# Kernel optimization log

Hardware: AMD Instinct MI355X
Metric: run time of the kernel (lower is better)

The kernel has to match this reference:

```python
import jax, jax.numpy as jnp
import numpy as np

H = 768
NH = 12
HD = H // NH
FF = 3072
E = 4
EPS = 1e-12


def _make_expert_params(key):
    ks = jax.random.split(key, 8)
    s = 0.02
    return {
        'wq': jax.random.normal(ks[0], (H, H), jnp.float32) * s,
        'wk': jax.random.normal(ks[1], (H, H), jnp.float32) * s,
        'wv': jax.random.normal(ks[2], (H, H), jnp.float32) * s,
        'wo': jax.random.normal(ks[3], (H, H), jnp.float32) * s,
        'bq': jnp.zeros((H,), jnp.float32),
        'bk': jnp.zeros((H,), jnp.float32),
        'bv': jnp.zeros((H,), jnp.float32),
        'bo': jnp.zeros((H,), jnp.float32),
        'ln1_g': jnp.ones((H,), jnp.float32),
        'ln1_b': jnp.zeros((H,), jnp.float32),
        'w1': jax.random.normal(ks[4], (H, FF), jnp.float32) * s,
        'b1': jnp.zeros((FF,), jnp.float32),
        'w2': jax.random.normal(ks[5], (FF, H), jnp.float32) * s,
        'b2': jnp.zeros((H,), jnp.float32),
        'ln2_g': jnp.ones((H,), jnp.float32),
        'ln2_b': jnp.zeros((H,), jnp.float32),
    }


def setup_inputs() -> dict:
    key = jax.random.key(0)
    k1, k2, kp = jax.random.split(key, 3)
    hidden_states = jax.random.normal(k1, (64, 128, H), jnp.float32)
    attention_mask = jnp.zeros((64, 128), jnp.float32)  # additive mask, 0 = attend
    centers = jax.random.normal(k2, (E, H), jnp.float32)
    pkeys = jax.random.split(kp, E)
    ps = [_make_expert_params(k) for k in pkeys]
    # stack expert params along leading axis for vectorized gather-by-expert
    params = {k: jnp.stack([p[k] for p in ps], axis=0) for k in ps[0]}
    out = {'hidden_states': hidden_states, 'attention_mask': attention_mask, 'centers': centers}
    out.update(params)
    return out


def _layernorm(x, g, b):
    mu = x.mean(-1, keepdims=True)
    var = ((x - mu) ** 2).mean(-1, keepdims=True)
    return (x - mu) * jax.lax.rsqrt(var + EPS) * g + b


def _encoder(x, mask, p):
    # x: [B,S,H], mask: [B,S] additive; p: per-sample expert params (leading dim B)
    B, S, _ = x.shape
    q = jnp.einsum('bsh,bhd->bsd', x, p['wq']) + p['bq'][:, None, :]
    k = jnp.einsum('bsh,bhd->bsd', x, p['wk']) + p['bk'][:, None, :]
    v = jnp.einsum('bsh,bhd->bsd', x, p['wv']) + p['bv'][:, None, :]
    q = q.reshape(B, S, NH, HD)
    k = k.reshape(B, S, NH, HD)
    v = v.reshape(B, S, NH, HD)
    scores = jnp.einsum('bqnd,bknd->bnqk', q, k) / np.sqrt(HD).astype(np.float32)
    scores = scores + mask[:, None, None, :]
    attn = jax.nn.softmax(scores, axis=-1)
    ctx = jnp.einsum('bnqk,bknd->bqnd', attn, v).reshape(B, S, H)
    att_out = jnp.einsum('bsh,bhd->bsd', ctx, p['wo']) + p['bo'][:, None, :]
    att_out = _layernorm(att_out + x, p['ln1_g'][:, None, :], p['ln1_b'][:, None, :])
    ffn = jnp.einsum('bsh,bhf->bsf', att_out, p['w1']) + p['b1'][:, None, :]
    ffn = jax.nn.gelu(ffn)
    ffn = jnp.einsum('bsf,bfh->bsh', ffn, p['w2']) + p['b2'][:, None, :]
    out = _layernorm(att_out + ffn, p['ln2_g'][:, None, :], p['ln2_b'][:, None, :])
    return out


def reference(hidden_states, attention_mask, centers,
              wq, wk, wv, wo, bq, bk, bv, bo, ln1_g, ln1_b,
              w1, b1, w2, b2, ln2_g, ln2_b):
    # routing: mean over seq, cdist to centers, argmin -> per-sentence expert id
    h_pca = hidden_states.mean(axis=1)  # [B,H]
    d2 = (jnp.sum(h_pca ** 2, -1, keepdims=True)
          - 2.0 * h_pca @ centers.T
          + jnp.sum(centers ** 2, -1)[None, :])
    eid = jnp.argmin(d2, axis=1)  # [B]
    params = {'wq': wq, 'wk': wk, 'wv': wv, 'wo': wo, 'bq': bq, 'bk': bk,
              'bv': bv, 'bo': bo, 'ln1_g': ln1_g, 'ln1_b': ln1_b,
              'w1': w1, 'b1': b1, 'w2': w2, 'b2': b2,
              'ln2_g': ln2_g, 'ln2_b': ln2_b}
    # gather per-sample expert params (jit-friendly, honors hard routing)
    psel = {k: v[eid] for k, v in params.items()}
    return _encoder(hidden_states, attention_mask, psel)
```

## Files before the change

kernel.cpp:

```cpp
#include <hip/hip_runtime.h>
#include <hip/hip_bf16.h>
#include <math.h>

#define HDIM 768
#define NHEAD 12
#define HEADD 64
#define FFDIM 3072
#define NEXP 4
#define SEQ 128
#define NB 64
#define QKVN 2304

typedef __attribute__((ext_vector_type(8))) _Float16 f16x8;
typedef __attribute__((ext_vector_type(4))) _Float16 f16x4;
typedef __attribute__((ext_vector_type(4))) float f32x4;

__device__ __forceinline__ float gelu_fast(float x) {
  float t = -1.5957691216057308f * x * __builtin_fmaf(0.044715f * x, x, 1.0f);
  return x * __builtin_amdgcn_rcpf(1.0f + __expf(t));
}

__device__ __forceinline__ void gld_lds16(const void* g, void* l) {
  __builtin_amdgcn_global_load_lds(
      (const __attribute__((address_space(1))) unsigned int*)g,
      (__attribute__((address_space(3))) unsigned int*)l, 16, 0, 0);
}

__global__ __launch_bounds__(256) void route_cvt_kernel(
    const float* __restrict__ hs, const float* __restrict__ centers,
    int* __restrict__ eid, _Float16* __restrict__ x16) {
  int b = blockIdx.x, t = threadIdx.x;
  __shared__ float hp[HDIM];
  __shared__ float dist[NEXP];
  const float* xb = hs + (size_t)b * SEQ * HDIM;
  _Float16* ob = x16 + (size_t)b * SEQ * HDIM;

  if (t < 192) {
    float p0 = 0.f, p1 = 0.f, p2 = 0.f, p3 = 0.f;
    for (int sq = 0; sq < SEQ; ++sq) {
      float4 v = ((const float4*)(xb + (size_t)sq * HDIM))[t];
      p0 += v.x; p1 += v.y; p2 += v.z; p3 += v.w;
      f16x4 h = {(_Float16)v.x, (_Float16)v.y, (_Float16)v.z, (_Float16)v.w};
      *(f16x4*)(ob + (size_t)sq * HDIM + t * 4) = h;
    }
    hp[t * 4 + 0] = p0 * (1.0f / SEQ);
    hp[t * 4 + 1] = p1 * (1.0f / SEQ);
    hp[t * 4 + 2] = p2 * (1.0f / SEQ);
    hp[t * 4 + 3] = p3 * (1.0f / SEQ);
  }
  if (t < NEXP) dist[t] = 0.f;
  __syncthreads();

  float pe[NEXP] = {0.f, 0.f, 0.f, 0.f};
  for (int h = t; h < HDIM; h += 256) {
    float v = hp[h];
#pragma unroll
    for (int e = 0; e < NEXP; ++e) {
      float d = v - centers[e * HDIM + h];
      pe[e] += d * d;
    }
  }
#pragma unroll
  for (int e = 0; e < NEXP; ++e) atomicAdd(&dist[e], pe[e]);
  __syncthreads();
  if (t == 0) {
    int best = 0; float bv = dist[0];
    for (int e = 1; e < NEXP; ++e) if (dist[e] < bv) { bv = dist[e]; best = e; }
    eid[b] = best;
  }
}

__device__ __forceinline__ void tr_tile(const float* __restrict__ ip,
                                        _Float16* __restrict__ op,
                                        int K, int N, int nb, int kb,
                                        float (*tile)[33], int t) {
  int tx = t & 31, ty = t >> 5;
  for (int i = ty; i < 32; i += 8)
    tile[i][tx] = ip[(size_t)(kb + i) * N + nb + tx];
  __syncthreads();
  for (int i = ty; i < 32; i += 8)
    op[(size_t)(nb + i) * K + kb + tx] = (_Float16)tile[tx][i];
}

__global__ __launch_bounds__(256) void prep_weights(
    const float* __restrict__ wq, const float* __restrict__ wk,
    const float* __restrict__ wv, const float* __restrict__ wo,
    const float* __restrict__ w1, const float* __restrict__ w2,
    const float* __restrict__ bq, const float* __restrict__ bk,
    const float* __restrict__ bv,
    _Float16* __restrict__ Wqkvt, _Float16* __restrict__ Wot,
    _Float16* __restrict__ W1t, _Float16* __restrict__ W2t,
    float* __restrict__ bqkv, const int* __restrict__ eid,
    int* __restrict__ order, int* __restrict__ ord_eid) {
  __shared__ float tile[32][33];
  int x = blockIdx.x, e = blockIdx.y, t = threadIdx.x;

  if (x < 1728) {
    int which = x / 576, local = x % 576;
    const float* src = (which == 0) ? wq : (which == 1) ? wk : wv;
    tr_tile(src + (size_t)e * HDIM * HDIM,
            Wqkvt + (size_t)which * HDIM * HDIM + (size_t)e * QKVN * HDIM,
            HDIM, HDIM, (local % 24) * 32, (local / 24) * 32, tile, t);
  } else if (x < 2304) {
    int local = x - 1728;
    tr_tile(wo + (size_t)e * HDIM * HDIM, Wot + (size_t)e * HDIM * HDIM,
            HDIM, HDIM, (local % 24) * 32, (local / 24) * 32, tile, t);
  } else if (x < 4608) {
    int local = x - 2304;
    tr_tile(w1 + (size_t)e * HDIM * FFDIM, W1t + (size_t)e * FFDIM * HDIM,
            HDIM, FFDIM, (local % 96) * 32, (local / 96) * 32, tile, t);
  } else if (x < 6912) {
    int local = x - 4608;
    tr_tile(w2 + (size_t)e * FFDIM * HDIM, W2t + (size_t)e * HDIM * FFDIM,
            FFDIM, HDIM, (local % 24) * 32, (local / 24) * 32, tile, t);
  } else if (x < 6948) {
    if (e == 0) {
      int i = (x - 6912) * 256 + t;
      if (i < NEXP * QKVN) {
        int ee = i / QKVN, n = i % QKVN;
        float v = (n < HDIM) ? bq[ee * HDIM + n]
                : (n < 2 * HDIM) ? bk[ee * HDIM + n - HDIM]
                                 : bv[ee * HDIM + n - 2 * HDIM];
        bqkv[i] = v;
      }
    }
  } else {
    if (e == 0 && t == 0) {
      int n = 0;
      for (int ee = 0; ee < NEXP; ++ee)
        for (int b = 0; b < NB; ++b)
          if (eid[b] == ee) { order[n] = b; ord_eid[n] = ee; n++; }
    }
  }
}

template <int OUT_F16, int GELU, int KDIM, int SPLITK>
__global__ __launch_bounds__(256, 2) void gemm_mfma(
    const _Float16* __restrict__ A, const _Float16* __restrict__ Wt,
    const float* __restrict__ Ball, const int* __restrict__ order,
    const int* __restrict__ ord_eid, void* __restrict__ Cv, int N) {
  constexpr int K = KDIM;
  constexpr int Kp = KDIM / SPLITK;
  constexpr int NIT = Kp / 32;
  int GX = N >> 8;
  int L = blockIdx.x;
  int low3 = L & 7, Mq = L >> 3;
  int x = Mq % GX, zhi = Mq / GX;
  int z = zhi * 8 + low3;
  int b = order[z];
  int e = ord_eid[z];
  int col0 = x * 256;
  int kz = blockIdx.y;
  int kbeg = kz * Kp;

  int t = threadIdx.x;
  int lane = t & 63, w = t >> 6;
  int quad = lane >> 4, l16 = lane & 15;
  int wc = w * 64;

  __shared__ __align__(16) _Float16 As[2 * 128 * 32];
  __shared__ __align__(16) _Float16 Bs[2 * 256 * 32];

  int ksw = ((t & 3) ^ ((t >> 2) & 3) ^ ((t >> 4) & 3)) * 8;
  int r0 = t >> 2;

  const _Float16* Ab = A + (size_t)b * SEQ * K + kbeg;
  const _Float16* Wb = Wt + (size_t)e * N * K + (size_t)col0 * K + kbeg;
  const _Float16* ga0 = Ab + (size_t)r0 * K + ksw;
  const _Float16* gb0 = Wb + (size_t)r0 * K + ksw;

  auto issue = [&](int c, int st) {
    int off = c * 32;
    _Float16* Ast = As + st * 4096;
    _Float16* Bst = Bs + st * 8192;
    gld_lds16(ga0 + off, Ast + t * 8);
    gld_lds16(ga0 + 64 * K + off, Ast + 2048 + t * 8);
    gld_lds16(gb0 + off, Bst + t * 8);
    gld_lds16(gb0 + 64 * K + off, Bst + 2048 + t * 8);
    gld_lds16(gb0 + 128 * K + off, Bst + 4096 + t * 8);
    gld_lds16(gb0 + 192 * K + off, Bst + 6144 + t * 8);
  };

  f32x4 acc[8][4];
#pragma unroll
  for (int i = 0; i < 8; ++i)
#pragma unroll
    for (int j = 0; j < 4; ++j) acc[i][j] = (f32x4){0.f, 0.f, 0.f, 0.f};

  int sl = (l16 & 3) ^ ((l16 >> 2) & 3);
  int kread = (quad ^ sl) * 8;

  issue(0, 0);

#pragma unroll 2
  for (int it = 0; it < NIT; ++it) {
    __builtin_amdgcn_s_waitcnt(0xF70);
    __builtin_amdgcn_s_barrier();
    if (it + 1 < NIT) issue(it + 1, (it + 1) & 1);

    int st = it & 1;
    const _Float16* Ast = As + st * 4096;
    const _Float16* Bst = Bs + st * 8192;
    f16x8 af[8], bf[4];
#pragma unroll
    for (int i = 0; i < 8; ++i)
      af[i] = *(const f16x8*)&Ast[(i * 16 + l16) * 32 + kread];
#pragma unroll
    for (int j = 0; j < 4; ++j)
      bf[j] = *(const f16x8*)&Bst[(wc + j * 16 + l16) * 32 + kread];
#pragma unroll
    for (int i = 0; i < 8; ++i)
#pragma unroll
      for (int j = 0; j < 4; ++j)
        acc[i][j] = __builtin_amdgcn_mfma_f32_16x16x32_f16(af[i], bf[j], acc[i][j], 0, 0, 0);
  }

  const float* bias = Ball + (size_t)e * N;

  if (OUT_F16) {
    _Float16* Ch = (_Float16*)Cv + (size_t)b * SEQ * N;
#pragma unroll
    for (int i = 0; i < 8; ++i)
#pragma unroll
      for (int j = 0; j < 4; ++j) {
        int col = col0 + wc + j * 16 + l16;
        float bv = bias[col];
#pragma unroll
        for (int r = 0; r < 4; ++r) {
          int row = i * 16 + quad * 4 + r;
          float v = acc[i][j][r] + bv;
          if (GELU) v = gelu_fast(v);
          Ch[(size_t)row * N + col] = (_Float16)v;
        }
      }
  } else {
    float* Cf = (float*)Cv + (size_t)kz * NB * SEQ * N + (size_t)b * SEQ * N;
    float bscale = (kz == 0) ? 1.f : 0.f;
#pragma unroll
    for (int i = 0; i < 8; ++i)
#pragma unroll
      for (int j = 0; j < 4; ++j) {
        int col = col0 + wc + j * 16 + l16;
        float bv = bias[col] * bscale;
#pragma unroll
        for (int r = 0; r < 4; ++r) {
          int row = i * 16 + quad * 4 + r;
          Cf[(size_t)row * N + col] = acc[i][j][r] + bv;
        }
      }
  }
}

__global__ __launch_bounds__(256) void attn_mfma(
    const _Float16* __restrict__ QKV, const float* __restrict__ mask,
    _Float16* __restrict__ Ctx) {
  int h = blockIdx.x, b = blockIdx.y;
  int t = threadIdx.x;
  int w = t >> 6, lane = t & 63, quad = lane >> 4, l16 = lane & 15;

  __shared__ __align__(16) char smem[54784];
  _Float16* Qs = (_Float16*)smem;
  _Float16* Ks = (_Float16*)(smem + 18432);
  _Float16* Ps = (_Float16*)smem;
  _Float16* Vt = (_Float16*)(smem + 36864);
  float* mrow = (float*)(smem + 54272);

  const _Float16* Qb = QKV + (size_t)b * SEQ * QKVN + h * HEADD;
  const _Float16* Kb = Qb + HDIM;
  const _Float16* Vb = Qb + 2 * HDIM;

#pragma unroll
  for (int it = 0; it < 4; ++it) {
    int chunk = t + it * 256;
    int row = chunk >> 3, c = chunk & 7;
    *(f16x8*)&Qs[row * 72 + c * 8] = *(const f16x8*)(Qb + (size_t)row * QKVN + c * 8);
    *(f16x8*)&Ks[row * 72 + c * 8] = *(const f16x8*)(Kb + (size_t)row * QKVN + c * 8);
  }
  {
    int vc = t & 7, vjp0 = t >> 3;
#pragma unroll
    for (int it = 0; it < 2; ++it) {
      int jp = vjp0 + it * 32;
      f16x8 v0 = *(const f16x8*)(Vb + (size_t)(2 * jp) * QKVN + vc * 8);
      f16x8 v1 = *(const f16x8*)(Vb + (size_t)(2 * jp + 1) * QKVN + vc * 8);
#pragma unroll
      for (int i = 0; i < 8; ++i) {
        int d = vc * 8 + i;
        unsigned ua = __builtin_bit_cast(unsigned short, (_Float16)v0[i]);
        unsigned ub = __builtin_bit_cast(unsigned short, (_Float16)v1[i]);
        ((unsigned*)Vt)[d * 68 + jp] = ua | (ub << 16);
      }
    }
  }
  if (t < SEQ) mrow[t] = mask[(size_t)b * SEQ + t];
  __syncthreads();

  int m0 = w * 32;
  f32x4 accs[2][8];
#pragma unroll
  for (int i = 0; i < 2; ++i)
#pragma unroll
    for (int j = 0; j < 8; ++j) accs[i][j] = (f32x4){0.f, 0.f, 0.f, 0.f};

#pragma unroll
  for (int ks = 0; ks < 2; ++ks) {
    int k0 = ks * 32 + quad * 8;
    f16x8 af[2], bf[8];
#pragma unroll
    for (int i = 0; i < 2; ++i)
      af[i] = *(const f16x8*)&Qs[(m0 + i * 16 + l16) * 72 + k0];
#pragma unroll
    for (int j = 0; j < 8; ++j)
      bf[j] = *(const f16x8*)&Ks[(j * 16 + l16) * 72 + k0];
#pragma unroll
    for (int i = 0; i < 2; ++i)
#pragma unroll
      for (int j = 0; j < 8; ++j)
        accs[i][j] = __builtin_amdgcn_mfma_f32_16x16x32_f16(af[i], bf[j], accs[i][j], 0, 0, 0);
  }
  __syncthreads();

  float mv[8];
#pragma unroll
  for (int j = 0; j < 8; ++j) mv[j] = mrow[j * 16 + l16];

  float linv[2][4];
#pragma unroll
  for (int i = 0; i < 2; ++i) {
#pragma unroll
    for (int j = 0; j < 8; ++j)
#pragma unroll
      for (int r = 0; r < 4; ++r)
        accs[i][j][r] = accs[i][j][r] * 0.125f + mv[j];
#pragma unroll
    for (int r = 0; r < 4; ++r) {
      float m = accs[i][0][r];
#pragma unroll
      for (int j = 1; j < 8; ++j) m = fmaxf(m, accs[i][j][r]);
      m = fmaxf(m, __shfl_xor(m, 1));
      m = fmaxf(m, __shfl_xor(m, 2));
      m = fmaxf(m, __shfl_xor(m, 4));
      m = fmaxf(m, __shfl_xor(m, 8));
      float sum = 0.f;
#pragma unroll
      for (int j = 0; j < 8; ++j) {
        float p = __expf(accs[i][j][r] - m);
        accs[i][j][r] = p;
        sum += p;
      }
      sum += __shfl_xor(sum, 1);
      sum += __shfl_xor(sum, 2);
      sum += __shfl_xor(sum, 4);
      sum += __shfl_xor(sum, 8);
      linv[i][r] = 1.f / sum;
    }
    int rowb = m0 + i * 16 + quad * 4;
#pragma unroll
    for (int j = 0; j < 8; ++j)
#pragma unroll
      for (int r = 0; r < 4; ++r)
        Ps[(rowb + r) * 136 + j * 16 + l16] = (_Float16)accs[i][j][r];
  }
  __syncthreads();

  f32x4 acco[2][4];
#pragma unroll
  for (int i = 0; i < 2; ++i)
#pragma unroll
    for (int j = 0; j < 4; ++j) acco[i][j] = (f32x4){0.f, 0.f, 0.f, 0.f};

#pragma unroll
  for (int ks = 0; ks < 4; ++ks) {
    int k0 = ks * 32 + quad * 8;
    f16x8 pa[2], vf[4];
#pragma unroll
    for (int i = 0; i < 2; ++i)
      pa[i] = *(const f16x8*)&Ps[(m0 + i * 16 + l16) * 136 + k0];
#pragma unroll
    for (int j = 0; j < 4; ++j)
      vf[j] = *(const f16x8*)&Vt[(j * 16 + l16) * 136 + k0];
#pragma unroll
    for (int i = 0; i < 2; ++i)
#pragma unroll
      for (int j = 0; j < 4; ++j)
        acco[i][j] = __builtin_amdgcn_mfma_f32_16x16x32_f16(pa[i], vf[j], acco[i][j], 0, 0, 0);
  }

  _Float16* Cb = Ctx + (size_t)b * SEQ * HDIM + h * HEADD;
#pragma unroll
  for (int i = 0; i < 2; ++i)
#pragma unroll
    for (int j = 0; j < 4; ++j)
#pragma unroll
      for (int r = 0; r < 4; ++r) {
        int row = m0 + i * 16 + quad * 4 + r;
        int d = j * 16 + l16;
        Cb[(size_t)row * HDIM + d] = (_Float16)(acco[i][j][r] * linv[i][r]);
      }
}

template <int NP>
__global__ __launch_bounds__(256) void resid_ln_kernel(
    const float* __restrict__ X, const float* __restrict__ P0,
    const float* __restrict__ P1,
    const float* __restrict__ Gall, const float* __restrict__ Ball,
    const int* __restrict__ eid, float* __restrict__ Out,
    _Float16* __restrict__ Out16) {
  int row = blockIdx.x, b = blockIdx.y, t = threadIdx.x;
  int e = eid[b];
  size_t off = ((size_t)b * SEQ + row) * HDIM;
  const float* x = X + off;
  const float* p0 = P0 + off;
  const float* p1 = (NP > 1) ? P1 + off : nullptr;
  float* o = Out + off;
  const float* g = Gall + (size_t)e * HDIM;
  const float* bb = Ball + (size_t)e * HDIM;

  __shared__ float buf[HDIM];
  __shared__ float red[256];

  float s = 0.f;
  for (int h = t; h < HDIM; h += 256) {
    float v = x[h] + p0[h];
    if (NP > 1) v += p1[h];
    buf[h] = v;
    s += v;
  }
  red[t] = s;
  __syncthreads();
  for (int off2 = 128; off2 > 0; off2 >>= 1) {
    if (t < off2) red[t] += red[t + off2];
    __syncthreads();
  }
  float mean = red[0] * (1.0f / HDIM);
  __syncthreads();

  float s2 = 0.f;
  for (int h = t; h < HDIM; h += 256) {
    float d = buf[h] - mean;
    s2 += d * d;
  }
  red[t] = s2;
  __syncthreads();
  for (int off2 = 128; off2 > 0; off2 >>= 1) {
    if (t < off2) red[t] += red[t + off2];
    __syncthreads();
  }
  float var = red[0] * (1.0f / HDIM);
  float rs = rsqrtf(var + 1e-12f);

  for (int h = t; h < HDIM; h += 256) {
    float v = (buf[h] - mean) * rs * g[h] + bb[h];
    o[h] = v;
    if (Out16) Out16[off + h] = (_Float16)v;
  }
}

extern "C" void kernel_launch(void* const* d_in, const int* in_sizes, int n_in,
                              void* d_out, int out_size, void* d_ws, size_t ws_size,
                              hipStream_t stream) {
  const float* hs   = (const float*)d_in[0];
  const float* mask = (const float*)d_in[1];
  const float* cen  = (const float*)d_in[2];
  const float* wq = (const float*)d_in[3];
  const float* wk = (const float*)d_in[4];
  const float* wv = (const float*)d_in[5];
  const float* wo = (const float*)d_in[6];
  const float* bq = (const float*)d_in[7];
  const float* bk = (const float*)d_in[8];
  const float* bv = (const float*)d_in[9];
  const float* bo = (const float*)d_in[10];
  const float* ln1g = (const float*)d_in[11];
  const float* ln1b = (const float*)d_in[12];
  const float* w1 = (const float*)d_in[13];
  const float* b1 = (const float*)d_in[14];
  const float* w2 = (const float*)d_in[15];
  const float* b2 = (const float*)d_in[16];
  const float* ln2g = (const float*)d_in[17];
  const float* ln2b = (const float*)d_in[18];
  float* out = (float*)d_out;

  const size_t sh = (size_t)SEQ * HDIM;

  char* p = (char*)d_ws;
  int* eid = (int*)p;                 p += 256;
  int* order = (int*)p;               p += 256;
  int* ord_eid = (int*)p;             p += 256;
  float* bqkv = (float*)p;            p += (size_t)NEXP * QKVN * 4;
  _Float16* Wqkvt = (_Float16*)p;     p += (size_t)NEXP * QKVN * HDIM * 2;
  _Float16* Wot = (_Float16*)p;       p += (size_t)NEXP * HDIM * HDIM * 2;
  _Float16* W1t = (_Float16*)p;       p += (size_t)NEXP * FFDIM * HDIM * 2;
  _Float16* W2t = (_Float16*)p;       p += (size_t)NEXP * HDIM * FFDIM * 2;
  _Float16* x16 = (_Float16*)p;       p += (size_t)NB * sh * 2;

  char* region = p;                   p += (size_t)NB * SEQ * QKVN * 2;
  _Float16* ctx16 = (_Float16*)p;     p += (size_t)NB * sh * 2;
  float* aof = (float*)p;             p += (size_t)NB * sh * 4;
  _Float16* ao16 = (_Float16*)p;      p += (size_t)NB * sh * 2;
  char* ffreg = p;                    p += (size_t)NB * SEQ * FFDIM * 2;

  float* woparts = (float*)ffreg;
  float* w2parts = (float*)region;
  _Float16* ff16 = (_Float16*)ffreg;

  route_cvt_kernel<<<NB, 256, 0, stream>>>(hs, cen, eid, x16);
  prep_weights<<<dim3(6949, NEXP), 256, 0, stream>>>(
      wq, wk, wv, wo, w1, w2, bq, bk, bv,
      Wqkvt, Wot, W1t, W2t, bqkv, eid, order, ord_eid);
  gemm_mfma<1, 0, HDIM, 1><<<dim3((QKVN / 256) * NB, 1), 256, 0, stream>>>(
      x16, Wqkvt, bqkv, order, ord_eid, region, QKVN);
  attn_mfma<<<dim3(NHEAD, NB), 256, 0, stream>>>(
      (const _Float16*)region, mask, ctx16);
  gemm_mfma<0, 0, HDIM, 2><<<dim3((HDIM / 256) * NB, 2), 256, 0, stream>>>(
      ctx16, Wot, bo, order, ord_eid, woparts, HDIM);
  resid_ln_kernel<2><<<dim3(SEQ, NB), 256, 0, stream>>>(
      hs, woparts, woparts + (size_t)NB * sh, ln1g, ln1b, eid, aof, ao16);
  gemm_mfma<1, 1, HDIM, 1><<<dim3((FFDIM / 256) * NB, 1), 256, 0, stream>>>(
      ao16, W1t, b1, order, ord_eid, ff16, FFDIM);
  gemm_mfma<0, 0, FFDIM, 2><<<dim3((HDIM / 256) * NB, 2), 256, 0, stream>>>(
      ff16, W2t, b2, order, ord_eid, w2parts, HDIM);
  resid_ln_kernel<2><<<dim3(SEQ, NB), 256, 0, stream>>>(
      aof, w2parts, w2parts + (size_t)NB * sh, ln2g, ln2b, eid, out,
      (_Float16*)nullptr);
}
```

Baseline: 484.6 us.

## Use 128x192 GEMM tiles with triple-buffered LDS and a new block-to-tile mapping

The grouped GEMM tile width drops from 256 to 192 columns, so each wave computes 48 columns. This gives more workgroups for the 256-CU device: for example 768/192=4 column tiles instead of 3, which helps wave quantisation. The LDS pipeline moves from double to triple buffering with a prefetch distance of 2, using partial vmcnt waits, to better hide global-to-LDS load latency. Block indices are remapped into a 1D grid that folds the split-K index in, interleaved in groups of 8, to change which workgroups run together for L2 reuse. In exchange, each tile has a lower MFMA-to-load ratio and uses more LDS per block (about 48KB), which may limit occupancy at 2 blocks per CU.

Result: no change. 484.4 us (-0.0%).

```diff
diff --git a/kernel.cpp b/kernel.cpp
--- a/kernel.cpp
+++ b/kernel.cpp
@@ -142,76 +142,78 @@
   constexpr int K = KDIM;
   constexpr int Kp = KDIM / SPLITK;
   constexpr int NIT = Kp / 32;
-  int GX = N >> 8;
+  int GX = N / 192;
+  int nwg = GX * NB * SPLITK;
   int L = blockIdx.x;
-  int low3 = L & 7, Mq = L >> 3;
-  int x = Mq % GX, zhi = Mq / GX;
-  int z = zhi * 8 + low3;
+  int r = (L & 7) * (nwg >> 3) + (L >> 3);
+  int z = r & 63;
+  int kz = (r >> 6) % SPLITK;
+  int c = (r >> 6) / SPLITK;
   int b = order[z];
   int e = ord_eid[z];
-  int col0 = x * 256;
-  int kz = blockIdx.y;
+  int col0 = c * 192;
   int kbeg = kz * Kp;
 
   int t = threadIdx.x;
   int lane = t & 63, w = t >> 6;
   int quad = lane >> 4, l16 = lane & 15;
-  int wc = w * 64;
-
-  __shared__ __align__(16) _Float16 As[2 * 128 * 32];
-  __shared__ __align__(16) _Float16 Bs[2 * 256 * 32];
+  int wc = w * 48;
+
+  __shared__ __align__(16) _Float16 As[3 * 128 * 32];
+  __shared__ __align__(16) _Float16 Bs[3 * 192 * 32];
 
   int ksw = ((t & 3) ^ ((t >> 2) & 3) ^ ((t >> 4) & 3)) * 8;
   int r0 = t >> 2;
 
   const _Float16* Ab = A + (size_t)b * SEQ * K + kbeg;
   const _Float16* Wb = Wt + (size_t)e * N * K + (size_t)col0 * K + kbeg;
-  const _Float16* ga0 = Ab + (size_t)r0 * K + ksw;
-  const _Float16* gb0 = Wb + (size_t)r0 * K + ksw;
-
-  auto issue = [&](int c, int st) {
-    int off = c * 32;
+  const _Float16* ga = Ab + (size_t)r0 * K + ksw;
+  const _Float16* gb = Wb + (size_t)r0 * K + ksw;
+
+  auto issue = [&](int cc, int st) {
+    int off = cc * 32;
     _Float16* Ast = As + st * 4096;
-    _Float16* Bst = Bs + st * 8192;
-    gld_lds16(ga0 + off, Ast + t * 8);
-    gld_lds16(ga0 + 64 * K + off, Ast + 2048 + t * 8);
-    gld_lds16(gb0 + off, Bst + t * 8);
-    gld_lds16(gb0 + 64 * K + off, Bst + 2048 + t * 8);
-    gld_lds16(gb0 + 128 * K + off, Bst + 4096 + t * 8);
-    gld_lds16(gb0 + 192 * K + off, Bst + 6144 + t * 8);
+    _Float16* Bst = Bs + st * 6144;
+    gld_lds16(ga + off,           Ast + t * 8);
+    gld_lds16(ga + 64 * K + off,  Ast + 2048 + t * 8);
+    gld_lds16(gb + off,           Bst + t * 8);
+    gld_lds16(gb + 64 * K + off,  Bst + 2048 + t * 8);
+    gld_lds16(gb + 128 * K + off, Bst + 4096 + t * 8);
   };
 
-  f32x4 acc[8][4];
+  f32x4 acc[8][3];
 #pragma unroll
   for (int i = 0; i < 8; ++i)
 #pragma unroll
-    for (int j = 0; j < 4; ++j) acc[i][j] = (f32x4){0.f, 0.f, 0.f, 0.f};
+    for (int j = 0; j < 3; ++j) acc[i][j] = (f32x4){0.f, 0.f, 0.f, 0.f};
 
   int sl = (l16 & 3) ^ ((l16 >> 2) & 3);
   int kread = (quad ^ sl) * 8;
 
   issue(0, 0);
-
-#pragma unroll 2
+  if (NIT > 1) issue(1, 1);
+
+#pragma unroll 3
   for (int it = 0; it < NIT; ++it) {
-    __builtin_amdgcn_s_waitcnt(0xF70);
+    if (it < NIT - 1) __builtin_amdgcn_s_waitcnt(0xF75);
+    else              __builtin_amdgcn_s_waitcnt(0xF70);
     __builtin_amdgcn_s_barrier();
-    if (it + 1 < NIT) issue(it + 1, (it + 1) & 1);
-
-    int st = it & 1;
+    if (it + 2 < NIT) issue(it + 2, (it + 2) % 3);
+
+    int st = it % 3;
     const _Float16* Ast = As + st * 4096;
-    const _Float16* Bst = Bs + st * 8192;
-    f16x8 af[8], bf[4];
+    const _Float16* Bst = Bs + st * 6144;
+    f16x8 af[8], bf[3];
 #pragma unroll
     for (int i = 0; i < 8; ++i)
       af[i] = *(const f16x8*)&Ast[(i * 16 + l16) * 32 + kread];
 #pragma unroll
-    for (int j = 0; j < 4; ++j)
+    for (int j = 0; j < 3; ++j)
       bf[j] = *(const f16x8*)&Bst[(wc + j * 16 + l16) * 32 + kread];
 #pragma unroll
     for (int i = 0; i < 8; ++i)
 #pragma unroll
-      for (int j = 0; j < 4; ++j)
+      for (int j = 0; j < 3; ++j)
         acc[i][j] = __builtin_amdgcn_mfma_f32_16x16x32_f16(af[i], bf[j], acc[i][j], 0, 0, 0);
   }
 
@@ -222,13 +224,13 @@
 #pragma unroll
     for (int i = 0; i < 8; ++i)
 #pragma unroll
-      for (int j = 0; j < 4; ++j) {
+      for (int j = 0; j < 3; ++j) {
         int col = col0 + wc + j * 16 + l16;
         float bv = bias[col];
 #pragma unroll
-        for (int r = 0; r < 4; ++r) {
-          int row = i * 16 + quad * 4 + r;
-          float v = acc[i][j][r] + bv;
+        for (int r2 = 0; r2 < 4; ++r2) {
+          int row = i * 16 + quad * 4 + r2;
+          float v = acc[i][j][r2] + bv;
           if (GELU) v = gelu_fast(v);
           Ch[(size_t)row * N + col] = (_Float16)v;
         }
@@ -239,13 +241,13 @@
 #pragma unroll
     for (int i = 0; i < 8; ++i)
 #pragma unroll
-      for (int j = 0; j < 4; ++j) {
+      for (int j = 0; j < 3; ++j) {
         int col = col0 + wc + j * 16 + l16;
         float bv = bias[col] * bscale;
 #pragma unroll
-        for (int r = 0; r < 4; ++r) {
-          int row = i * 16 + quad * 4 + r;
-          Cf[(size_t)row * N + col] = acc[i][j][r] + bv;
+        for (int r2 = 0; r2 < 4; ++r2) {
+          int row = i * 16 + quad * 4 + r2;
+          Cf[(size_t)row * N + col] = acc[i][j][r2] + bv;
         }
       }
   }
@@ -507,17 +509,17 @@
   prep_weights<<<dim3(6949, NEXP), 256, 0, stream>>>(
       wq, wk, wv, wo, w1, w2, bq, bk, bv,
       Wqkvt, Wot, W1t, W2t, bqkv, eid, order, ord_eid);
-  gemm_mfma<1, 0, HDIM, 1><<<dim3((QKVN / 256) * NB, 1), 256, 0, stream>>>(
+  gemm_mfma<1, 0, HDIM, 1><<<dim3((QKVN / 192) * NB, 1), 256, 0, stream>>>(
       x16, Wqkvt, bqkv, order, ord_eid, region, QKVN);
   attn_mfma<<<dim3(NHEAD, NB), 256, 0, stream>>>(
       (const _Float16*)region, mask, ctx16);
-  gemm_mfma<0, 0, HDIM, 2><<<dim3((HDIM / 256) * NB, 2), 256, 0, stream>>>(
+  gemm_mfma<0, 0, HDIM, 2><<<dim3((HDIM / 192) * NB * 2, 1), 256, 0, stream>>>(
       ctx16, Wot, bo, order, ord_eid, woparts, HDIM);
   resid_ln_kernel<2><<<dim3(SEQ, NB), 256, 0, stream>>>(
       hs, woparts, woparts + (size_t)NB * sh, ln1g, ln1b, eid, aof, ao16);
-  gemm_mfma<1, 1, HDIM, 1><<<dim3((FFDIM / 256) * NB, 1), 256, 0, stream>>>(
+  gemm_mfma<1, 1, HDIM, 1><<<dim3((FFDIM / 192) * NB, 1), 256, 0, stream>>>(
       ao16, W1t, b1, order, ord_eid, ff16, FFDIM);
-  gemm_mfma<0, 0, FFDIM, 2><<<dim3((HDIM / 256) * NB, 2), 256, 0, stream>>>(
+  gemm_mfma<0, 0, FFDIM, 2><<<dim3((HDIM / 192) * NB * 2, 1), 256, 0, stream>>>(
       ff16, W2t, b2, order, ord_eid, w2parts, HDIM);
   resid_ln_kernel<2><<<dim3(SEQ, NB), 256, 0, stream>>>(
       aof, w2parts, w2parts + (size_t)NB * sh, ln2g, ln2b, eid, out,
```
